# Performance work log

Measured on AMD Instinct MI355X. Metric: run time of the kernel, lower is better.

Reference implementation:

```python
import jax, jax.numpy as jnp
import numpy as np

B, IN, OUT, R, G = 1024, 4096, 4096, 16, 16
N_GROUPS = IN * OUT // G  # 1048576


def setup_inputs() -> dict:
    key = jax.random.key(0)
    k1, k2, k3, k4, k5 = jax.random.split(key, 5)
    x = jax.random.normal(k1, (B, IN), dtype=jnp.float32)
    # packed 4-bit weights: each int holds two nibbles (low | high<<4), values 0..255
    qweight = jax.random.randint(k2, (N_GROUPS, G // 2), 0, 256, dtype=jnp.int32)
    # positive per-group scale (original stores abs-max as fp16, used as fp32)
    scale_factor = jax.random.uniform(k3, (N_GROUPS, 1), dtype=jnp.float32, minval=0.01, maxval=1.0)
    # kaiming-normal-ish init for lora_a; lora_b nonzero for a non-degenerate baseline
    lora_a = jax.random.normal(k4, (R, IN), dtype=jnp.float32) * np.sqrt(2.0 / IN).astype(np.float32)
    lora_b = jax.random.normal(k5, (OUT, R), dtype=jnp.float32) * 0.01
    alpha = jnp.ones((1,), dtype=jnp.float32)
    return {"x": x, "qweight": qweight, "scale_factor": scale_factor,
            "lora_a": lora_a, "lora_b": lora_b, "alpha": alpha}


def _dequantize_4bit(qweight, scale_factor):
    # qweight: [n_groups, G/2] int32 packed nibbles; scale: [n_groups, 1]
    g, half = qweight.shape
    lo = qweight & 15            # even positions
    hi = (qweight >> 4) & 15     # odd positions
    q8 = jnp.stack([lo, hi], axis=-1).reshape(g, half * 2)  # interleave -> [n_groups, G]
    x_norm = q8.astype(jnp.float32) / 15.0
    return x_norm * 2.0 * scale_factor - scale_factor       # [n_groups, G]


def reference(x, qweight, scale_factor, lora_a, lora_b, alpha):
    # dequantize and view as (in_features, -1), matching weight.view(x.shape[1], -1)
    weight = _dequantize_4bit(qweight, scale_factor).reshape(x.shape[1], -1)  # [IN, OUT]
    base = jnp.einsum('bi,oi->bo', x, weight)  # F.linear(x, weight) = x @ weight.T
    lora = alpha * jnp.einsum('br,or->bo', jnp.einsum('bi,ri->br', x, lora_a), lora_b)
    return base + lora
```

## Files before the change

### kernel.cpp

```cpp
#include <hip/hip_runtime.h>

typedef __attribute__((ext_vector_type(2))) _Float16 h2;
typedef __attribute__((ext_vector_type(2))) __fp16 p2;
typedef __attribute__((ext_vector_type(8))) _Float16 f16x8;
typedef __attribute__((ext_vector_type(4))) float fv4;
typedef __attribute__((ext_vector_type(4))) int iv4;
typedef __attribute__((ext_vector_type(2))) int iv2;
typedef unsigned int u32;

#define K_IN 4096
#define N_OUT 4096
#define NG 520


__global__ __launch_bounds__(256) void prep_one(
        const float* __restrict__ x, const float* __restrict__ la,
        const int* __restrict__ qw, const float* __restrict__ sc,
        const float* __restrict__ lb, const float* __restrict__ alphap,
        _Float16* __restrict__ Wp, _Float16* __restrict__ xp)
{
    __shared__ __align__(16) char lsm[16640];
    int bid = blockIdx.x;
    int t = threadIdx.x;

    if (bid < 1024) {
        float (*red)[16] = (float (*)[16])(lsm + 16384);
        int b = bid, rb = b >> 4, rl = b & 15;
        const fv4* xp4 = (const fv4*)(x + (size_t)b * K_IN);
        fv4 xv[4];
#pragma unroll
        for (int j = 0; j < 4; ++j) xv[j] = xp4[t + j * 256];
        float acc[16];
#pragma unroll
        for (int r = 0; r < 16; ++r) {
            const fv4* ap = (const fv4*)(la + (size_t)r * K_IN);
            float s = 0.f;
#pragma unroll
            for (int j = 0; j < 4; ++j) {
                fv4 av = ap[t + j * 256];
                s = fmaf(xv[j].x, av.x, s);
                s = fmaf(xv[j].y, av.y, s);
                s = fmaf(xv[j].z, av.z, s);
                s = fmaf(xv[j].w, av.w, s);
            }
            acc[r] = s;
        }
#pragma unroll
        for (int r = 0; r < 16; ++r) {
#pragma unroll
            for (int off = 1; off < 64; off <<= 1)
                acc[r] += __shfl_xor(acc[r], off);
        }
        int lane = t & 63, w = t >> 6;
        if (lane < 16) red[w][lane] = acc[lane];
        __syncthreads();
        if (t < 8) {
            int gl = t;
            union { p2 h[4]; iv4 v; } u;
            u.v = iv4{0, 0, 0, 0};
            if (gl < 2) {
#pragma unroll
                for (int e2 = 0; e2 < 4; ++e2) {
                    int k0 = gl * 8 + e2 * 2;
                    float v0 = red[0][k0] + red[1][k0] + red[2][k0] + red[3][k0];
                    float v1 = red[0][k0+1] + red[1][k0+1] + red[2][k0+1] + red[3][k0+1];
                    u.h[e2] = __builtin_amdgcn_cvt_pkrtz(v0, v1);
                }
            }
            *(iv4*)(xp + (((size_t)rb * NG + 512 + gl) * 16 + rl) * 8) = u.v;
        }
    } else if (bid < 1280) {
        int cb = bid - 1024;
        int o_l = t >> 4, gi_l = t & 15;
#pragma unroll 1
        for (int chunk = 0; chunk < 8; ++chunk) {
#pragma unroll
            for (int i = 0; i < 2; ++i) {
                int gi = chunk * 32 + i * 16 + gi_l;
                int o = cb * 16 + o_l;
                const int* qp = qw + ((size_t)o * 256 + gi) * 8;
                iv4 q0 = *(const iv4*)qp;
                iv4 q1 = *(const iv4*)(qp + 4);
                float s = sc[(size_t)o * 256 + gi];
                _Float16 c0h = (_Float16)(s * (2.0f / 15.0f));
                _Float16 c1h = (_Float16)(-s);
                h2 c0 = {c0h, c0h}, c1 = {c1h, c1h};
                h2 m1024 = {(_Float16)-1024.f, (_Float16)-1024.f};
                union { h2 h[4]; iv4 v; } w0, w1;
                int vals[8] = {q0.x, q0.y, q0.z, q0.w, q1.x, q1.y, q1.z, q1.w};
#pragma unroll
                for (int e = 0; e < 8; ++e) {
                    unsigned wv = (unsigned)vals[e];
                    unsigned qb = (wv & 15u) | ((wv & 0xF0u) << 12) | 0x64006400u;
                    h2 qh;
                    __builtin_memcpy(&qh, &qb, 4);
                    h2 r = (qh + m1024) * c0 + c1;
                    if (e < 4) w0.h[e] = r; else w1.h[e - 4] = r;
                }
                int gl0 = i * 32 + 2 * gi_l;
                int s0 = o_l ^ gi_l;
                *(iv4*)(lsm + (gl0 * 16 + s0) * 16) = w0.v;
                *(iv4*)(lsm + ((gl0 + 1) * 16 + s0) * 16) = w1.v;
            }
            __syncthreads();
#pragma unroll
            for (int i = 0; i < 4; ++i) {
                int s_ = t + i * 256;
                int gl = s_ >> 4, oo = s_ & 15;
                iv4 v = *(const iv4*)(lsm + (gl * 16 + (oo ^ ((gl >> 1) & 15))) * 16);
                *(iv4*)(Wp + (((size_t)cb * NG + chunk * 64) * 16 + s_) * 8) = v;
            }
            __syncthreads();
        }
        if (t < 128) {
            int gl = t >> 4, rl = t & 15;
            int o = cb * 16 + rl;
            union { p2 h[4]; iv4 v; } u;
            u.v = iv4{0, 0, 0, 0};
            if (gl < 2) {
                float al = alphap[0];
                const float* wp = lb + (size_t)o * 16 + gl * 8;
#pragma unroll
                for (int e = 0; e < 4; ++e)
                    u.h[e] = __builtin_amdgcn_cvt_pkrtz(al * wp[2 * e], al * wp[2 * e + 1]);
            }
            *(iv4*)(Wp + (((size_t)cb * NG + 512 + gl) * 16 + rl) * 8) = u.v;
        }
    } else {
        int q2 = bid - 1280;
        int rb = q2 >> 2, kq = q2 & 3;
        int row = t >> 4, q = t & 15;
#pragma unroll 1
        for (int chunk = 0; chunk < 2; ++chunk) {
            int base_k = kq * 1024 + chunk * 512;
#pragma unroll
            for (int i = 0; i < 8; ++i) {
                int quad = q + i * 16;
                const float* p = x + (size_t)(rb * 16 + row) * K_IN + base_k + quad * 4;
                fv4 v = *(const fv4*)p;
                union { p2 h[2]; iv2 vv; } u;
                u.h[0] = __builtin_amdgcn_cvt_pkrtz(v.x, v.y);
                u.h[1] = __builtin_amdgcn_cvt_pkrtz(v.z, v.w);
                int gl = quad >> 1, sub = quad & 1;
                *(iv2*)(lsm + (gl * 16 + (row ^ (gl & 15))) * 16 + sub * 8) = u.vv;
            }
            __syncthreads();
#pragma unroll
            for (int i = 0; i < 4; ++i) {
                int s_ = t + i * 256;
                int gl = s_ >> 4, rr = s_ & 15;
                iv4 v = *(const iv4*)(lsm + (gl * 16 + (rr ^ (gl & 15))) * 16);
                *(iv4*)(xp + (((size_t)rb * NG + kq * 128 + chunk * 64) * 16 + s_) * 8) = v;
            }
            __syncthreads();
        }
    }
}

__global__ __launch_bounds__(512, 1) void qlora_gemm2(
        const _Float16* __restrict__ xp, const _Float16* __restrict__ Wp,
        float* __restrict__ out)
{
    __shared__ __align__(16) char lds[65536];

    int bid = blockIdx.x;
    int xcd = bid & 7, j = bid >> 3;
    int by = j & 7, bx = xcd * 4 + (j >> 3);
    int bm0 = by << 7, bn0 = bx << 7;

    int t = threadIdx.x;
    int lane = t & 63;
    int wid = t >> 6;
    int kg = wid & 1, wn = (wid >> 1) & 1, wm = wid >> 2;
    int rl = lane & 15, hq = lane >> 4;

    const char* abase[4];
    const char* bbase[4];
#pragma unroll
    for (int m = 0; m < 4; ++m) {
        int rb = by * 8 + wm * 4 + m;
        abase[m] = (const char*)xp + (((size_t)rb * NG + kg * 4 + hq) * 16 + rl) * 16;
    }
#pragma unroll
    for (int n = 0; n < 4; ++n) {
        int cb = bx * 8 + wn * 4 + n;
        bbase[n] = (const char*)Wp + (((size_t)cb * NG + kg * 4 + hq) * 16 + rl) * 16;
    }

    struct Frag { iv4 a[4]; iv4 b[4]; };
    Frag fA, fB;

    auto LOADF = [&](Frag& f, int ts) {
        size_t off = (size_t)ts * 2048;
#pragma unroll
        for (int m = 0; m < 4; ++m) f.a[m] = *(const iv4*)(abase[m] + off);
#pragma unroll
        for (int n = 0; n < 4; ++n) f.b[n] = *(const iv4*)(bbase[n] + off);
    };

    fv4 acc[4][4];
#pragma unroll
    for (int m = 0; m < 4; ++m)
#pragma unroll
        for (int n = 0; n < 4; ++n)
            acc[m][n] = fv4{0.f, 0.f, 0.f, 0.f};

    auto MFMAF = [&](const Frag& f) {
        union { iv4 v; f16x8 h; } ua[4], ub[4];
#pragma unroll
        for (int m = 0; m < 4; ++m) ua[m].v = f.a[m];
#pragma unroll
        for (int n = 0; n < 4; ++n) ub[n].v = f.b[n];
        __builtin_amdgcn_s_setprio(1);
#pragma unroll
        for (int m = 0; m < 4; ++m)
#pragma unroll
            for (int n = 0; n < 4; ++n)
                acc[m][n] = __builtin_amdgcn_mfma_f32_16x16x32_f16(
                    ua[m].h, ub[n].h, acc[m][n], 0, 0, 0);
        __builtin_amdgcn_s_setprio(0);
    };

    LOADF(fA, 0);
#pragma unroll 1
    for (int ts = 0; ts < 64; ts += 2) {
        LOADF(fB, ts + 1);
        MFMAF(fA);
        LOADF(fA, ts + 2);
        MFMAF(fB);
    }
    MFMAF(fA);

    __syncthreads();
    if (kg == 1) {
        char* dmp = lds + (wm * 2 + wn) * 16384;
#pragma unroll
        for (int m = 0; m < 4; ++m)
#pragma unroll
            for (int n = 0; n < 4; ++n)
                *(fv4*)(dmp + (m * 4 + n) * 1024 + lane * 16) = acc[m][n];
    }
    __syncthreads();
    if (kg == 0) {
        const char* dmp = lds + (wm * 2 + wn) * 16384;
#pragma unroll
        for (int m = 0; m < 4; ++m) {
            int row0 = bm0 + wm * 64 + m * 16 + hq * 4;
#pragma unroll
            for (int n = 0; n < 4; ++n) {
                fv4 p = *(const fv4*)(dmp + (m * 4 + n) * 1024 + lane * 16);
                fv4 v = acc[m][n];
                v.x += p.x; v.y += p.y; v.z += p.z; v.w += p.w;
                int col = bn0 + wn * 64 + n * 16 + rl;
#pragma unroll
                for (int r = 0; r < 4; ++r)
                    out[(size_t)(row0 + r) * N_OUT + col] = v[r];
            }
        }
    }
}

extern "C" void kernel_launch(void* const* d_in, const int* in_sizes, int n_in,
                              void* d_out, int out_size, void* d_ws, size_t ws_size,
                              hipStream_t stream) {
    const float* x  = (const float*)d_in[0];
    const int*   qw = (const int*)d_in[1];
    const float* sc = (const float*)d_in[2];
    const float* la = (const float*)d_in[3];
    const float* lb = (const float*)d_in[4];
    const float* al = (const float*)d_in[5];
    float* out = (float*)d_out;

    const size_t WP_BYTES = (size_t)256 * NG * 16 * 16;
    _Float16* Wp = (_Float16*)d_ws;
    _Float16* xp = (_Float16*)((char*)d_ws + WP_BYTES);
    (void)ws_size; (void)n_in; (void)in_sizes; (void)out_size;

    prep_one<<<1536, 256, 0, stream>>>(x, la, qw, sc, lb, al, Wp, xp);
    qlora_gemm2<<<256, 512, 0, stream>>>(xp, Wp, out);
}
```

Baseline: 77.82 us.

## Drop split-K warps in GEMM, widen per-warp K, split weight prep blocks

The GEMM no longer splits K across two warp groups. It now runs 256 threads per block, and each warp covers the full K range with double-width fragments, which removes the LDS reduction and its two barriers. Scheduling group barriers are added to interleave the global loads with the MFMAs. The weight-dequant part of prep is split four ways across more blocks to raise parallelism in that phase. The price is half as many waves per CU in the GEMM, giving less latency hiding, plus higher register pressure from the 8-wide fragments.

```diff
diff --git a/kernel.cpp b/kernel.cpp
--- a/kernel.cpp
+++ b/kernel.cpp
@@ -69,11 +69,13 @@
             }
             *(iv4*)(xp + (((size_t)rb * NG + 512 + gl) * 16 + rl) * 8) = u.v;
         }
-    } else if (bid < 1280) {
-        int cb = bid - 1024;
+    } else if (bid < 2048) {
+        int idx = bid - 1024;
+        int cb = idx >> 2, part = idx & 3;
+        int c0 = part * 2;
         int o_l = t >> 4, gi_l = t & 15;
 #pragma unroll 1
-        for (int chunk = 0; chunk < 8; ++chunk) {
+        for (int chunk = c0; chunk < c0 + 2; ++chunk) {
 #pragma unroll
             for (int i = 0; i < 2; ++i) {
                 int gi = chunk * 32 + i * 16 + gi_l;
@@ -84,7 +86,7 @@
                 float s = sc[(size_t)o * 256 + gi];
                 _Float16 c0h = (_Float16)(s * (2.0f / 15.0f));
                 _Float16 c1h = (_Float16)(-s);
-                h2 c0 = {c0h, c0h}, c1 = {c1h, c1h};
+                h2 c0v = {c0h, c0h}, c1v = {c1h, c1h};
                 h2 m1024 = {(_Float16)-1024.f, (_Float16)-1024.f};
                 union { h2 h[4]; iv4 v; } w0, w1;
                 int vals[8] = {q0.x, q0.y, q0.z, q0.w, q1.x, q1.y, q1.z, q1.w};
@@ -94,7 +96,7 @@
                     unsigned qb = (wv & 15u) | ((wv & 0xF0u) << 12) | 0x64006400u;
                     h2 qh;
                     __builtin_memcpy(&qh, &qb, 4);
-                    h2 r = (qh + m1024) * c0 + c1;
+                    h2 r = (qh + m1024) * c0v + c1v;
                     if (e < 4) w0.h[e] = r; else w1.h[e - 4] = r;
                 }
                 int gl0 = i * 32 + 2 * gi_l;
@@ -112,7 +114,7 @@
             }
             __syncthreads();
         }
-        if (t < 128) {
+        if (part == 0 && t < 128) {
             int gl = t >> 4, rl = t & 15;
             int o = cb * 16 + rl;
             union { p2 h[4]; iv4 v; } u;
@@ -127,7 +129,7 @@
             *(iv4*)(Wp + (((size_t)cb * NG + 512 + gl) * 16 + rl) * 8) = u.v;
         }
     } else {
-        int q2 = bid - 1280;
+        int q2 = bid - 2048;
         int rb = q2 >> 2, kq = q2 & 3;
         int row = t >> 4, q = t & 15;
 #pragma unroll 1
@@ -157,12 +159,10 @@
     }
 }
 
-__global__ __launch_bounds__(512, 1) void qlora_gemm2(
+__global__ __launch_bounds__(256, 1) void qlora_gemm2(
         const _Float16* __restrict__ xp, const _Float16* __restrict__ Wp,
         float* __restrict__ out)
 {
-    __shared__ __align__(16) char lds[65536];
-
     int bid = blockIdx.x;
     int xcd = bid & 7, j = bid >> 3;
     int by = j & 7, bx = xcd * 4 + (j >> 3);
@@ -171,7 +171,7 @@
     int t = threadIdx.x;
     int lane = t & 63;
     int wid = t >> 6;
-    int kg = wid & 1, wn = (wid >> 1) & 1, wm = wid >> 2;
+    int wm = wid >> 1, wn = wid & 1;
     int rl = lane & 15, hq = lane >> 4;
 
     const char* abase[4];
@@ -179,23 +179,28 @@
 #pragma unroll
     for (int m = 0; m < 4; ++m) {
         int rb = by * 8 + wm * 4 + m;
-        abase[m] = (const char*)xp + (((size_t)rb * NG + kg * 4 + hq) * 16 + rl) * 16;
+        abase[m] = (const char*)xp + (((size_t)rb * NG + hq) * 16 + rl) * 16;
     }
 #pragma unroll
     for (int n = 0; n < 4; ++n) {
         int cb = bx * 8 + wn * 4 + n;
-        bbase[n] = (const char*)Wp + (((size_t)cb * NG + kg * 4 + hq) * 16 + rl) * 16;
-    }
-
-    struct Frag { iv4 a[4]; iv4 b[4]; };
+        bbase[n] = (const char*)Wp + (((size_t)cb * NG + hq) * 16 + rl) * 16;
+    }
+
+    struct Frag { iv4 a[8]; iv4 b[8]; };
     Frag fA, fB;
 
     auto LOADF = [&](Frag& f, int ts) {
         size_t off = (size_t)ts * 2048;
 #pragma unroll
-        for (int m = 0; m < 4; ++m) f.a[m] = *(const iv4*)(abase[m] + off);
-#pragma unroll
-        for (int n = 0; n < 4; ++n) f.b[n] = *(const iv4*)(bbase[n] + off);
+        for (int s2 = 0; s2 < 2; ++s2) {
+#pragma unroll
+            for (int m = 0; m < 4; ++m)
+                f.a[s2 * 4 + m] = *(const iv4*)(abase[m] + off + s2 * 1024);
+#pragma unroll
+            for (int n = 0; n < 4; ++n)
+                f.b[s2 * 4 + n] = *(const iv4*)(bbase[n] + off + s2 * 1024);
+        }
     };
 
     fv4 acc[4][4];
@@ -206,18 +211,21 @@
             acc[m][n] = fv4{0.f, 0.f, 0.f, 0.f};
 
     auto MFMAF = [&](const Frag& f) {
-        union { iv4 v; f16x8 h; } ua[4], ub[4];
-#pragma unroll
-        for (int m = 0; m < 4; ++m) ua[m].v = f.a[m];
-#pragma unroll
-        for (int n = 0; n < 4; ++n) ub[n].v = f.b[n];
         __builtin_amdgcn_s_setprio(1);
 #pragma unroll
-        for (int m = 0; m < 4; ++m)
-#pragma unroll
-            for (int n = 0; n < 4; ++n)
-                acc[m][n] = __builtin_amdgcn_mfma_f32_16x16x32_f16(
-                    ua[m].h, ub[n].h, acc[m][n], 0, 0, 0);
+        for (int s2 = 0; s2 < 2; ++s2) {
+            union { iv4 v; f16x8 h; } ua[4], ub[4];
+#pragma unroll
+            for (int m = 0; m < 4; ++m) ua[m].v = f.a[s2 * 4 + m];
+#pragma unroll
+            for (int n = 0; n < 4; ++n) ub[n].v = f.b[s2 * 4 + n];
+#pragma unroll
+            for (int m = 0; m < 4; ++m)
+#pragma unroll
+                for (int n = 0; n < 4; ++n)
+                    acc[m][n] = __builtin_amdgcn_mfma_f32_16x16x32_f16(
+                        ua[m].h, ub[n].h, acc[m][n], 0, 0, 0);
+        }
         __builtin_amdgcn_s_setprio(0);
     };
 
@@ -225,37 +233,25 @@
 #pragma unroll 1
     for (int ts = 0; ts < 64; ts += 2) {
         LOADF(fB, ts + 1);
+        __builtin_amdgcn_sched_group_barrier(0x20, 16, 0);
         MFMAF(fA);
+        __builtin_amdgcn_sched_group_barrier(0x8, 32, 0);
         LOADF(fA, ts + 2);
+        __builtin_amdgcn_sched_group_barrier(0x20, 16, 0);
         MFMAF(fB);
+        __builtin_amdgcn_sched_group_barrier(0x8, 32, 0);
     }
     MFMAF(fA);
 
-    __syncthreads();
-    if (kg == 1) {
-        char* dmp = lds + (wm * 2 + wn) * 16384;
-#pragma unroll
-        for (int m = 0; m < 4; ++m)
-#pragma unroll
-            for (int n = 0; n < 4; ++n)
-                *(fv4*)(dmp + (m * 4 + n) * 1024 + lane * 16) = acc[m][n];
-    }
-    __syncthreads();
-    if (kg == 0) {
-        const char* dmp = lds + (wm * 2 + wn) * 16384;
-#pragma unroll
-        for (int m = 0; m < 4; ++m) {
-            int row0 = bm0 + wm * 64 + m * 16 + hq * 4;
-#pragma unroll
-            for (int n = 0; n < 4; ++n) {
-                fv4 p = *(const fv4*)(dmp + (m * 4 + n) * 1024 + lane * 16);
-                fv4 v = acc[m][n];
-                v.x += p.x; v.y += p.y; v.z += p.z; v.w += p.w;
-                int col = bn0 + wn * 64 + n * 16 + rl;
-#pragma unroll
-                for (int r = 0; r < 4; ++r)
-                    out[(size_t)(row0 + r) * N_OUT + col] = v[r];
-            }
+#pragma unroll
+    for (int m = 0; m < 4; ++m) {
+        int row0 = bm0 + wm * 64 + m * 16 + hq * 4;
+#pragma unroll
+        for (int n = 0; n < 4; ++n) {
+            int col = bn0 + wn * 64 + n * 16 + rl;
+#pragma unroll
+            for (int r = 0; r < 4; ++r)
+                out[(size_t)(row0 + r) * N_OUT + col] = acc[m][n][r];
         }
     }
 }
@@ -276,6 +272,6 @@
     _Float16* xp = (_Float16*)((char*)d_ws + WP_BYTES);
     (void)ws_size; (void)n_in; (void)in_sizes; (void)out_size;
 
-    prep_one<<<1536, 256, 0, stream>>>(x, la, qw, sc, lb, al, Wp, xp);
-    qlora_gemm2<<<256, 512, 0, stream>>>(xp, Wp, out);
+    prep_one<<<2304, 256, 0, stream>>>(x, la, qw, sc, lb, al, Wp, xp);
+    qlora_gemm2<<<256, 256, 0, stream>>>(xp, Wp, out);
 }
```

Result: faster. 75.39 us (-3.1%).
